# Performance work log

Hardware: AMD Instinct MI355X
Metric: run time of the kernel (lower is better)

The kernel has to match this reference:

```python
import jax, jax.numpy as jnp
import numpy as np

T, N, E = 6, 50000, 1600000
NFEAT, NHID, NCLASS = 256, 256, 16
SLOPE = 11.0 / 48.0  # eval-mode RReLU: mean of default (lower=1/8, upper=1/3)


def _grcu(H_seq, src, dst, val, Wz, Uz, bz, Wr, Ur, br, Wh, Uh, bh, Q0):
    """One GRCU layer: matrix-GRU weight evolution + sparse GCN aggregation per step.
    H_seq: [T, N, in]  src/dst: [T, E] int  val: [T, E]  Q0: [in, out]."""
    n = H_seq.shape[1]

    def step(Q, xs):
        H, s, d, v = xs
        # mat_GRU_cell: x = hidden = prev_Q (z_topk path is unused in this repo's forward)
        z = jax.nn.sigmoid(Wz @ Q + Uz @ Q + bz)
        r = jax.nn.sigmoid(Wr @ Q + Ur @ Q + br)
        h = jnp.tanh(Wh @ Q + Uh @ (r * Q) + bh)
        Qn = (1.0 - z) * Q + z * h
        XW = H @ Qn                                   # [N, out]
        msg = v[:, None] * XW[s]                      # per-edge gather: Ahat row weights
        agg = jax.ops.segment_sum(msg, d, num_segments=n)  # Ahat @ (H @ Qn)
        out = jnp.where(agg >= 0, agg, SLOPE * agg)   # RReLU (eval)
        return Qn, out

    _, out_seq = jax.lax.scan(step, Q0, (H_seq, src, dst, val))
    return out_seq  # [T, N, out]


def setup_inputs() -> dict:
    key = jax.random.key(0)
    ks = iter(jax.random.split(key, 64))

    def rn(shape, scale=0.05):
        return jax.random.normal(next(ks), shape, dtype=jnp.float32) * scale

    inp = {
        "node_feats": jax.random.normal(next(ks), (T, N, NFEAT), dtype=jnp.float32),
        "edge_val": jax.random.uniform(next(ks), (T, E), dtype=jnp.float32),
    }
    for l, (fi, fo) in enumerate([(NFEAT, NHID), (NHID, NHID)]):
        for g in ("z", "r", "h"):
            inp[f"l{l}_W{g}"] = rn((fi, fi))
            inp[f"l{l}_U{g}"] = rn((fi, fi))
            inp[f"l{l}_b{g}"] = jnp.zeros((fi, fo), dtype=jnp.float32)
        inp[f"l{l}_Q0"] = rn((fi, fo))
    inp["mlp_W1"] = rn((NHID, NHID))
    inp["mlp_b1"] = jnp.zeros((NHID,), dtype=jnp.float32)
    inp["mlp_W2"] = rn((NHID, NCLASS))
    inp["mlp_b2"] = jnp.zeros((NCLASS,), dtype=jnp.float32)
    inp["edge_src"] = jax.random.randint(next(ks), (T, E), 0, N, dtype=jnp.int32)
    inp["edge_dst"] = jax.random.randint(next(ks), (T, E), 0, N, dtype=jnp.int32)
    return inp


def reference(node_feats, edge_val,
              l0_Wz, l0_Uz, l0_bz, l0_Wr, l0_Ur, l0_br, l0_Wh, l0_Uh, l0_bh, l0_Q0,
              l1_Wz, l1_Uz, l1_bz, l1_Wr, l1_Ur, l1_br, l1_Wh, l1_Uh, l1_bh, l1_Q0,
              mlp_W1, mlp_b1, mlp_W2, mlp_b2,
              edge_src, edge_dst):
    h1 = _grcu(node_feats, edge_src, edge_dst, edge_val,
               l0_Wz, l0_Uz, l0_bz, l0_Wr, l0_Ur, l0_br, l0_Wh, l0_Uh, l0_bh, l0_Q0)
    h2 = _grcu(h1, edge_src, edge_dst, edge_val,
               l1_Wz, l1_Uz, l1_bz, l1_Wr, l1_Ur, l1_br, l1_Wh, l1_Uh, l1_bh, l1_Q0)
    out = h2[-1]                                    # last timestep, [N, nhid]
    hid = jax.nn.relu(out @ mlp_W1 + mlp_b1)
    logits = hid @ mlp_W2 + mlp_b2
    return jax.nn.log_softmax(logits, axis=1)       # [N, nclass]
```

## Files before the change

### kernel.cpp

```cpp
#include <hip/hip_runtime.h>
#include <cstddef>

#define SLOPE_F (11.0f / 48.0f)

static const int NN = 50000;
static const int EE = 1600000;
static const int D  = 256;
static const int NCH = 196;
static const int GB  = 391;

typedef __attribute__((ext_vector_type(8))) short short8;
typedef __attribute__((ext_vector_type(4))) float f32x4;

__device__ __forceinline__ ushort f2bf(float f) {
    unsigned u = __float_as_uint(f);
    unsigned r = (u + 0x7fffu + ((u >> 16) & 1u)) >> 16;
    return (ushort)r;
}
__device__ __forceinline__ float bf2f(ushort u) {
    return __uint_as_float(((unsigned)u) << 16);
}

__global__ __launch_bounds__(256) void prephist_kernel(
        const float* __restrict__ Wz0, const float* __restrict__ Uz0,
        const float* __restrict__ Wr0, const float* __restrict__ Ur0,
        const float* __restrict__ Wh0, const float* __restrict__ Uh0,
        const float* __restrict__ Wz1, const float* __restrict__ Uz1,
        const float* __restrict__ Wr1, const float* __restrict__ Ur1,
        const float* __restrict__ Wh1, const float* __restrict__ Uh1,
        const float* __restrict__ W1,
        float* __restrict__ TW, ushort* __restrict__ BtW1,
        const int* __restrict__ dst, int* __restrict__ deg) {
    int b = blockIdx.x;
    int tid = threadIdx.x;
    if (b >= 144) {
        int e = (b - 144) * 256 + tid;
        if (e < EE) atomicAdd(&deg[dst[e]], 1);
        return;
    }
    __shared__ float lt[64][65];
    if (b < 128) {
        int mat = b >> 4;
        int tr = (b >> 2) & 3, tc = b & 3;
        const float* P = nullptr; const float* S = nullptr;
        switch (mat) {
            case 0: P = Wz0; S = Uz0; break;
            case 1: P = Wr0; S = Ur0; break;
            case 2: P = Wh0; break;
            case 3: P = Uh0; break;
            case 4: P = Wz1; S = Uz1; break;
            case 5: P = Wr1; S = Ur1; break;
            case 6: P = Wh1; break;
            default: P = Uh1; break;
        }
#pragma unroll
        for (int r0 = 0; r0 < 64; r0 += 4) {
            int r = r0 + (tid >> 6);
            int c = tid & 63;
            int row = tr * 64 + r, col = tc * 64 + c;
            float v = P[row * 256 + col];
            if (S) v += S[row * 256 + col];
            lt[r][c] = v;
        }
        __syncthreads();
#pragma unroll
        for (int c0 = 0; c0 < 64; c0 += 4) {
            int c = c0 + (tid >> 6);
            int r = tid & 63;
            int row = tr * 64 + r, col = tc * 64 + c;
            TW[((size_t)mat * 256 + col) * 256 + row] = lt[r][c];
        }
    } else {
        int t = b - 128;
        int tr = (t >> 2) & 3, tc = t & 3;
#pragma unroll
        for (int r0 = 0; r0 < 64; r0 += 4) {
            int r = r0 + (tid >> 6);
            int c = tid & 63;
            lt[r][c] = W1[(tr * 64 + r) * 256 + tc * 64 + c];
        }
        __syncthreads();
#pragma unroll
        for (int c0 = 0; c0 < 64; c0 += 4) {
            int c = c0 + (tid >> 6);
            int r = tid & 63;
            BtW1[(size_t)(tc * 64 + c) * 256 + tr * 64 + r] = f2bf(lt[r][c]);
        }
    }
}

__global__ __launch_bounds__(256) void gruscan_kernel(
        const float* __restrict__ TW,
        const float* __restrict__ bz0, const float* __restrict__ br0,
        const float* __restrict__ bh0, const float* __restrict__ Q00,
        const float* __restrict__ bz1, const float* __restrict__ br1,
        const float* __restrict__ bh1, const float* __restrict__ Q01,
        ushort* __restrict__ Bt,
        const int* __restrict__ deg, int* __restrict__ rs, int* __restrict__ cur,
        int* __restrict__ bsum, int* __restrict__ boff, int* __restrict__ done) {
    int tid = threadIdx.x;
    if (blockIdx.x >= 128) {
        __shared__ int wsum[4];
        __shared__ int lastflag;
        int blk = blockIdx.x - 128;
        int i = blk * 256 + tid;
        int lane = tid & 63, wv = tid >> 6;
        int v = (i < NN) ? deg[i] : 0;
        int x = v;
#pragma unroll
        for (int off = 1; off < 64; off <<= 1) {
            int t = __shfl_up(x, off, 64);
            if (lane >= off) x += t;
        }
        if (lane == 63) wsum[wv] = x;
        __syncthreads();
        if (tid == 0) {
            int s = 0;
#pragma unroll
            for (int q = 0; q < 4; ++q) { int t = wsum[q]; wsum[q] = s; s += t; }
            bsum[blk] = s;
        }
        __syncthreads();
        if (i < NN) { int p = wsum[wv] + x - v; rs[i] = p; cur[i] = p; }
        __threadfence();
        if (tid == 0) lastflag = (atomicAdd(done, 1) == NCH - 1);
        __syncthreads();
        if (lastflag) {
            __threadfence();
            int bv = (tid < NCH) ? bsum[tid] : 0;
            int bx = bv;
#pragma unroll
            for (int off = 1; off < 64; off <<= 1) {
                int t = __shfl_up(bx, off, 64);
                if (lane >= off) bx += t;
            }
            if (lane == 63) wsum[wv] = bx;
            __syncthreads();
            if (tid == 0) {
                int s = 0;
#pragma unroll
                for (int q = 0; q < 4; ++q) { int t = wsum[q]; wsum[q] = s; s += t; }
            }
            __syncthreads();
            if (tid < NCH) boff[tid] = wsum[wv] + bx - bv;
        }
        return;
    }
    __shared__ float qs[256][4];
    __shared__ float rqs[256][4];
    int layer = blockIdx.x >> 6;
    int j0 = (blockIdx.x & 63) * 4;
    int i = tid;
    const float* MzT = TW + (size_t)layer * 4 * 65536;
    const float* MrT = MzT + 65536;
    const float* WhT = MzT + 2 * 65536;
    const float* UhT = MzT + 3 * 65536;
    const float* bz = layer ? bz1 : bz0;
    const float* br = layer ? br1 : br0;
    const float* bh = layer ? bh1 : bh0;
    const float* Q0 = layer ? Q01 : Q00;

    float4 bzv = *(const float4*)&bz[i * 256 + j0];
    float4 brv = *(const float4*)&br[i * 256 + j0];
    float4 bhv = *(const float4*)&bh[i * 256 + j0];
    float bza[4] = {bzv.x, bzv.y, bzv.z, bzv.w};
    float bra[4] = {brv.x, brv.y, brv.z, brv.w};
    float bha[4] = {bhv.x, bhv.y, bhv.z, bhv.w};

    float4 qv = *(const float4*)&Q0[i * 256 + j0];
    *(float4*)&qs[i][0] = qv;
    __syncthreads();

    float qn[4] = {qv.x, qv.y, qv.z, qv.w};
    for (int step = 0; step < 6; ++step) {
        float az[4] = {}, ar[4] = {}, ah[4] = {};
#pragma unroll 4
        for (int k = 0; k < 256; ++k) {
            float mz = MzT[k * 256 + i];
            float mr = MrT[k * 256 + i];
            float wh = WhT[k * 256 + i];
            float4 qk = *(const float4*)&qs[k][0];
            float qa[4] = {qk.x, qk.y, qk.z, qk.w};
#pragma unroll
            for (int c = 0; c < 4; ++c) {
                az[c] += mz * qa[c];
                ar[c] += mr * qa[c];
                ah[c] += wh * qa[c];
            }
        }
        float z[4], qo[4];
        float4 qown = *(const float4*)&qs[i][0];
        qo[0] = qown.x; qo[1] = qown.y; qo[2] = qown.z; qo[3] = qown.w;
        float rq[4];
#pragma unroll
        for (int c = 0; c < 4; ++c) {
            z[c] = 1.f / (1.f + expf(-(az[c] + bza[c])));
            float r = 1.f / (1.f + expf(-(ar[c] + bra[c])));
            rq[c] = r * qo[c];
        }
        float4 rqv; rqv.x = rq[0]; rqv.y = rq[1]; rqv.z = rq[2]; rqv.w = rq[3];
        *(float4*)&rqs[i][0] = rqv;
        __syncthreads();
        float bu[4] = {};
#pragma unroll 4
        for (int k = 0; k < 256; ++k) {
            float uh = UhT[k * 256 + i];
            float4 rk = *(const float4*)&rqs[k][0];
            float ra[4] = {rk.x, rk.y, rk.z, rk.w};
#pragma unroll
            for (int c = 0; c < 4; ++c) bu[c] += uh * ra[c];
        }
        float4 qnv;
#pragma unroll
        for (int c = 0; c < 4; ++c) {
            float h = tanhf(ah[c] + bu[c] + bha[c]);
            qn[c] = (1.f - z[c]) * qo[c] + z[c] * h;
        }
        qnv.x = qn[0]; qnv.y = qn[1]; qnv.z = qn[2]; qnv.w = qn[3];
        *(float4*)&qs[i][0] = qnv;
        __syncthreads();
    }
#pragma unroll
    for (int c = 0; c < 4; ++c)
        Bt[(size_t)layer * 65536 + (size_t)(j0 + c) * 256 + i] = f2bf(qn[c]);
}

template <int ASRC, int EPI>
__device__ __forceinline__ void gemm_body(int bid, int tid,
                                          const ushort* __restrict__ A,
                                          const float* __restrict__ Af,
                                          const ushort* __restrict__ Bt,
                                          const float* __restrict__ bias,
                                          ushort* __restrict__ C, int M) {
    int w = tid >> 6, l = tid & 63;
    int lr = l & 15;
    int lk = l >> 4;
    int row0 = bid * 128 + w * 32;
    int ra = row0 + lr;      if (ra > M - 1) ra = M - 1;
    int rb = row0 + 16 + lr; if (rb > M - 1) rb = M - 1;
    const ushort* Ap0  = A  + (size_t)ra * 256 + lk * 8;
    const ushort* Ap1  = A  + (size_t)rb * 256 + lk * 8;
    const float*  Apf0 = Af + (size_t)ra * 256 + lk * 8;
    const float*  Apf1 = Af + (size_t)rb * 256 + lk * 8;
    const ushort* Bp   = Bt + (size_t)lr * 256 + lk * 8;

    f32x4 acc0[16] = {};
    f32x4 acc1[16] = {};
#pragma unroll
    for (int kc = 0; kc < 8; ++kc) {
        short8 a0, a1;
        if (ASRC == 0) {
            a0 = *(const short8*)(Ap0 + kc * 32);
            a1 = *(const short8*)(Ap1 + kc * 32);
        } else {
            float4 f0 = *(const float4*)(Apf0 + kc * 32);
            float4 f1 = *(const float4*)(Apf0 + kc * 32 + 4);
            float4 g0 = *(const float4*)(Apf1 + kc * 32);
            float4 g1 = *(const float4*)(Apf1 + kc * 32 + 4);
            a0[0] = (short)f2bf(f0.x); a0[1] = (short)f2bf(f0.y);
            a0[2] = (short)f2bf(f0.z); a0[3] = (short)f2bf(f0.w);
            a0[4] = (short)f2bf(f1.x); a0[5] = (short)f2bf(f1.y);
            a0[6] = (short)f2bf(f1.z); a0[7] = (short)f2bf(f1.w);
            a1[0] = (short)f2bf(g0.x); a1[1] = (short)f2bf(g0.y);
            a1[2] = (short)f2bf(g0.z); a1[3] = (short)f2bf(g0.w);
            a1[4] = (short)f2bf(g1.x); a1[5] = (short)f2bf(g1.y);
            a1[6] = (short)f2bf(g1.z); a1[7] = (short)f2bf(g1.w);
        }
#pragma unroll
        for (int nb = 0; nb < 16; ++nb) {
            short8 bf = *(const short8*)(Bp + (size_t)nb * 4096 + kc * 32);
            acc0[nb] = __builtin_amdgcn_mfma_f32_16x16x32_bf16(a0, bf, acc0[nb], 0, 0, 0);
            acc1[nb] = __builtin_amdgcn_mfma_f32_16x16x32_bf16(a1, bf, acc1[nb], 0, 0, 0);
        }
    }

    int ro = lk * 4;
#pragma unroll
    for (int nb = 0; nb < 16; ++nb) {
        int gc = nb * 16 + lr;
        float bb = (EPI == 1) ? bias[gc] : 0.f;
#pragma unroll
        for (int q = 0; q < 4; ++q) {
            int g0 = row0 + ro + q;
            if (g0 < M) {
                float v = acc0[nb][q];
                if (EPI == 1) v = fmaxf(v + bb, 0.f);
                C[(size_t)g0 * 256 + gc] = f2bf(v);
            }
            int g1 = row0 + 16 + ro + q;
            if (g1 < M) {
                float v = acc1[nb][q];
                if (EPI == 1) v = fmaxf(v + bb, 0.f);
                C[(size_t)g1 * 256 + gc] = f2bf(v);
            }
        }
    }
}

template <int ASRC, int EPI>
__global__ __launch_bounds__(256) void gemm_mfma(const ushort* __restrict__ A,
                                                 const float* __restrict__ Af,
                                                 const ushort* __restrict__ Bt,
                                                 const float* __restrict__ bias,
                                                 ushort* __restrict__ C, int M) {
    gemm_body<ASRC, EPI>(blockIdx.x, threadIdx.x, A, Af, Bt, bias, C, M);
}

__global__ __launch_bounds__(256) void gemsca_kernel(const float* __restrict__ Af,
                                                     const ushort* __restrict__ Bt,
                                                     ushort* __restrict__ C, int M,
                                                     const int* __restrict__ src,
                                                     const int* __restrict__ dst,
                                                     const float* __restrict__ val,
                                                     int* __restrict__ cur,
                                                     const int* __restrict__ boff,
                                                     unsigned long long* __restrict__ csr) {
    if (blockIdx.x < GB) {
        gemm_body<1, 0>(blockIdx.x, threadIdx.x, nullptr, Af, Bt, nullptr, C, M);
        return;
    }
    int e = (blockIdx.x - GB) * 256 + threadIdx.x;
    if (e < EE) {
        int d = dst[e];
        int p = atomicAdd(&cur[d], 1) + boff[d >> 8];
        unsigned long long pk = (unsigned long long)(unsigned)src[e]
                              | ((unsigned long long)(unsigned)__float_as_uint(val[e]) << 32);
        __builtin_nontemporal_store(pk, &csr[p]);
    }
}

__global__ __launch_bounds__(256) void agg_csr_kernel(const ushort* __restrict__ XW,
                                                      const int2* __restrict__ csr,
                                                      const int* __restrict__ rs,
                                                      const int* __restrict__ boff,
                                                      ushort* __restrict__ out) {
    int d = blockIdx.x * 4 + (threadIdx.x >> 6);
    if (d >= NN) return;
    int l = threadIdx.x & 63;
    int h = l >> 5;
    int il = l & 31;
    int beg = rs[d] + boff[d >> 8];
    int end = (d + 1 < NN) ? (rs[d + 1] + boff[(d + 1) >> 8]) : EE;
    float a0 = 0.f, a1 = 0.f, a2 = 0.f, a3 = 0.f;
    float a4 = 0.f, a5 = 0.f, a6 = 0.f, a7 = 0.f;
    int i = beg + h;
    for (; i + 14 < end; i += 16) {
        int2 e[8];
        short8 x[8];
#pragma unroll
        for (int u = 0; u < 8; ++u) e[u] = csr[i + 2 * u];
#pragma unroll
        for (int u = 0; u < 8; ++u)
            x[u] = *(const short8*)&XW[(size_t)e[u].x * D + il * 8];
#pragma unroll
        for (int u = 0; u < 8; ++u) {
            float v = __int_as_float(e[u].y);
            a0 += v * bf2f((ushort)x[u][0]);
            a1 += v * bf2f((ushort)x[u][1]);
            a2 += v * bf2f((ushort)x[u][2]);
            a3 += v * bf2f((ushort)x[u][3]);
            a4 += v * bf2f((ushort)x[u][4]);
            a5 += v * bf2f((ushort)x[u][5]);
            a6 += v * bf2f((ushort)x[u][6]);
            a7 += v * bf2f((ushort)x[u][7]);
        }
    }
    for (; i + 6 < end; i += 8) {
        int2 e[4];
        short8 x[4];
#pragma unroll
        for (int u = 0; u < 4; ++u) e[u] = csr[i + 2 * u];
#pragma unroll
        for (int u = 0; u < 4; ++u)
            x[u] = *(const short8*)&XW[(size_t)e[u].x * D + il * 8];
#pragma unroll
        for (int u = 0; u < 4; ++u) {
            float v = __int_as_float(e[u].y);
            a0 += v * bf2f((ushort)x[u][0]);
            a1 += v * bf2f((ushort)x[u][1]);
            a2 += v * bf2f((ushort)x[u][2]);
            a3 += v * bf2f((ushort)x[u][3]);
            a4 += v * bf2f((ushort)x[u][4]);
            a5 += v * bf2f((ushort)x[u][5]);
            a6 += v * bf2f((ushort)x[u][6]);
            a7 += v * bf2f((ushort)x[u][7]);
        }
    }
    for (; i < end; i += 2) {
        int2 e0 = csr[i];
        float v0 = __int_as_float(e0.y);
        short8 x0 = *(const short8*)&XW[(size_t)e0.x * D + il * 8];
        a0 += v0 * bf2f((ushort)x0[0]); a1 += v0 * bf2f((ushort)x0[1]);
        a2 += v0 * bf2f((ushort)x0[2]); a3 += v0 * bf2f((ushort)x0[3]);
        a4 += v0 * bf2f((ushort)x0[4]); a5 += v0 * bf2f((ushort)x0[5]);
        a6 += v0 * bf2f((ushort)x0[6]); a7 += v0 * bf2f((ushort)x0[7]);
    }
    a0 += __shfl_xor(a0, 32); a1 += __shfl_xor(a1, 32);
    a2 += __shfl_xor(a2, 32); a3 += __shfl_xor(a3, 32);
    a4 += __shfl_xor(a4, 32); a5 += __shfl_xor(a5, 32);
    a6 += __shfl_xor(a6, 32); a7 += __shfl_xor(a7, 32);
    if (h == 0) {
        float r[8] = {a0, a1, a2, a3, a4, a5, a6, a7};
        short8 o;
#pragma unroll
        for (int c = 0; c < 8; ++c) {
            float v = r[c];
            v = (v >= 0.f) ? v : SLOPE_F * v;
            o[c] = (short)f2bf(v);
        }
        *(short8*)&out[(size_t)d * D + il * 8] = o;
    }
}

__global__ void mlp2_kernel(const ushort* __restrict__ hid, const float* __restrict__ W2,
                            const float* __restrict__ b2, float* __restrict__ out, int M) {
    int tid = threadIdx.x;
    int n = blockIdx.x * 16 + (tid >> 4);
    int c = tid & 15;
    if (n >= M) return;
    float acc = b2[c];
    const ushort* hp = hid + (size_t)n * D;
    for (int k = 0; k < D; k += 8) {
        short8 h8 = *(const short8*)(hp + k);
#pragma unroll
        for (int u = 0; u < 8; ++u)
            acc += bf2f((ushort)h8[u]) * W2[(k + u) * 16 + c];
    }
    float m = acc;
#pragma unroll
    for (int off = 1; off < 16; off <<= 1)
        m = fmaxf(m, __shfl_xor(m, off, 16));
    float ex = expf(acc - m);
    float s = ex;
#pragma unroll
    for (int off = 1; off < 16; off <<= 1)
        s += __shfl_xor(s, off, 16);
    out[(size_t)n * 16 + c] = acc - m - logf(s);
}

extern "C" void kernel_launch(void* const* d_in, const int* in_sizes, int n_in,
                              void* d_out, int out_size, void* d_ws, size_t ws_size,
                              hipStream_t stream) {
    const float* node_feats = (const float*)d_in[0];
    const float* edge_val   = (const float*)d_in[1];
    const float* l0_Wz = (const float*)d_in[2];
    const float* l0_Uz = (const float*)d_in[3];
    const float* l0_bz = (const float*)d_in[4];
    const float* l0_Wr = (const float*)d_in[5];
    const float* l0_Ur = (const float*)d_in[6];
    const float* l0_br = (const float*)d_in[7];
    const float* l0_Wh = (const float*)d_in[8];
    const float* l0_Uh = (const float*)d_in[9];
    const float* l0_bh = (const float*)d_in[10];
    const float* l0_Q0 = (const float*)d_in[11];
    const float* l1_Wz = (const float*)d_in[12];
    const float* l1_Uz = (const float*)d_in[13];
    const float* l1_bz = (const float*)d_in[14];
    const float* l1_Wr = (const float*)d_in[15];
    const float* l1_Ur = (const float*)d_in[16];
    const float* l1_br = (const float*)d_in[17];
    const float* l1_Wh = (const float*)d_in[18];
    const float* l1_Uh = (const float*)d_in[19];
    const float* l1_bh = (const float*)d_in[20];
    const float* l1_Q0 = (const float*)d_in[21];
    const float* W1 = (const float*)d_in[22];
    const float* b1 = (const float*)d_in[23];
    const float* W2 = (const float*)d_in[24];
    const float* b2 = (const float*)d_in[25];
    const int* e_src = (const int*)d_in[26];
    const int* e_dst = (const int*)d_in[27];
    float* out = (float*)d_out;

    const size_t BIG = (size_t)NN * D;
    ushort* XWb = (ushort*)d_ws;
    ushort* H   = XWb + BIG;
    ushort* Bt  = H + BIG;
    float*  TW  = (float*)(Bt + 3 * 65536);
    int2*   csr = (int2*)(TW + 8 * 65536);
    int*    deg = (int*)(csr + EE);
    int*    done = deg + NN;
    int*    rs  = done + 1;
    int*    cur = rs + NN;
    int*    bsum = cur + NN;
    int*    boff = bsum + 200;

    const float* feats5 = node_feats + (size_t)5 * BIG;
    const int*   src5   = e_src + (size_t)5 * EE;
    const int*   dst5   = e_dst + (size_t)5 * EE;
    const float* val5   = edge_val + (size_t)5 * EE;

    hipMemsetAsync(deg, 0, (NN + 1) * sizeof(int), stream);

    const int histblocks = (EE + 255) / 256;
    prephist_kernel<<<144 + histblocks, 256, 0, stream>>>(
        l0_Wz, l0_Uz, l0_Wr, l0_Ur, l0_Wh, l0_Uh,
        l1_Wz, l1_Uz, l1_Wr, l1_Ur, l1_Wh, l1_Uh,
        W1, TW, Bt + 2 * 65536, dst5, deg);

    gruscan_kernel<<<128 + NCH, 256, 0, stream>>>(TW, l0_bz, l0_br, l0_bh, l0_Q0,
                                                  l1_bz, l1_br, l1_bh, l1_Q0, Bt,
                                                  deg, rs, cur, bsum, boff, done);

    gemsca_kernel<<<GB + histblocks, 256, 0, stream>>>(feats5, Bt + 0 * 65536, XWb, NN,
                                                       src5, dst5, val5, cur, boff,
                                                       (unsigned long long*)csr);

    const int ablocks = (NN + 3) / 4;

    agg_csr_kernel<<<ablocks, 256, 0, stream>>>(XWb, csr, rs, boff, H);

    gemm_mfma<0, 0><<<GB, 256, 0, stream>>>(H, nullptr, Bt + 1 * 65536, nullptr, XWb, NN);
    agg_csr_kernel<<<ablocks, 256, 0, stream>>>(XWb, csr, rs, boff, H);

    gemm_mfma<0, 1><<<GB, 256, 0, stream>>>(H, nullptr, Bt + 2 * 65536, b1, XWb, NN);
    mlp2_kernel<<<(NN + 15) / 16, 256, 0, stream>>>(XWb, W2, b2, out, NN);
}
```

Baseline: 714.3 us.

## Rewrite matrix-GRU weight scan with bf16 MFMA and grid-wide barriers

The per-thread fp32 scalar FMA loops in the GRU weight-evolution kernel are replaced with 16x16x32 bf16 MFMA tiles. Each weight matrix is split into hi and lo bf16 halves so the weights keep roughly fp32 accuracy. The recurrent Q and r*Q state now live in global bf16 buffers and are exchanged between 128 blocks through a spin-wait grid barrier, two per step. The aim is to cut the latency-bound serial GRU phase. The cost is lower precision on the recurrent state and a reliance on all 128 GRU blocks being co-resident for the barrier.

```diff
diff --git a/kernel.cpp b/kernel.cpp
--- a/kernel.cpp
+++ b/kernel.cpp
@@ -29,19 +29,18 @@
         const float* __restrict__ Wr1, const float* __restrict__ Ur1,
         const float* __restrict__ Wh1, const float* __restrict__ Uh1,
         const float* __restrict__ W1,
-        float* __restrict__ TW, ushort* __restrict__ BtW1,
+        const float* __restrict__ Q00, const float* __restrict__ Q01,
+        ushort* __restrict__ WB, ushort* __restrict__ BtW1, ushort* __restrict__ Qt,
         const int* __restrict__ dst, int* __restrict__ deg) {
     int b = blockIdx.x;
     int tid = threadIdx.x;
-    if (b >= 144) {
-        int e = (b - 144) * 256 + tid;
+    if (b >= 112) {
+        int e = (b - 112) * 256 + tid;
         if (e < EE) atomicAdd(&deg[dst[e]], 1);
         return;
     }
-    __shared__ float lt[64][65];
-    if (b < 128) {
-        int mat = b >> 4;
-        int tr = (b >> 2) & 3, tc = b & 3;
+    if (b < 64) {
+        int mat = b >> 3;
         const float* P = nullptr; const float* S = nullptr;
         switch (mat) {
             case 0: P = Wz0; S = Uz0; break;
@@ -53,25 +52,22 @@
             case 6: P = Wh1; break;
             default: P = Uh1; break;
         }
-#pragma unroll
-        for (int r0 = 0; r0 < 64; r0 += 4) {
-            int r = r0 + (tid >> 6);
-            int c = tid & 63;
-            int row = tr * 64 + r, col = tc * 64 + c;
-            float v = P[row * 256 + col];
-            if (S) v += S[row * 256 + col];
-            lt[r][c] = v;
-        }
-        __syncthreads();
-#pragma unroll
-        for (int c0 = 0; c0 < 64; c0 += 4) {
-            int c = c0 + (tid >> 6);
-            int r = tid & 63;
-            int row = tr * 64 + r, col = tc * 64 + c;
-            TW[((size_t)mat * 256 + col) * 256 + row] = lt[r][c];
-        }
-    } else {
-        int t = b - 128;
+        size_t base = (size_t)mat * 2 * 65536;
+#pragma unroll 4
+        for (int u = 0; u < 32; ++u) {
+            int idx = (b & 7) * 8192 + u * 256 + tid;
+            float v = P[idx];
+            if (S) v += S[idx];
+            ushort hi = f2bf(v);
+            ushort lo = f2bf(v - bf2f(hi));
+            WB[base + idx] = hi;
+            WB[base + 65536 + idx] = lo;
+        }
+        return;
+    }
+    __shared__ float lt[64][65];
+    if (b < 80) {
+        int t = b - 64;
         int tr = (t >> 2) & 3, tc = t & 3;
 #pragma unroll
         for (int r0 = 0; r0 < 64; r0 += 4) {
@@ -86,16 +82,47 @@
             int r = tid & 63;
             BtW1[(size_t)(tc * 64 + c) * 256 + tr * 64 + r] = f2bf(lt[r][c]);
         }
-    }
-}
-
-__global__ __launch_bounds__(256) void gruscan_kernel(
-        const float* __restrict__ TW,
+    } else {
+        int t = b - 80;
+        int layer = t >> 4;
+        int tt = t & 15;
+        int tr = (tt >> 2) & 3, tc = tt & 3;
+        const float* Q0 = layer ? Q01 : Q00;
+#pragma unroll
+        for (int r0 = 0; r0 < 64; r0 += 4) {
+            int r = r0 + (tid >> 6);
+            int c = tid & 63;
+            lt[r][c] = Q0[(tr * 64 + r) * 256 + tc * 64 + c];
+        }
+        __syncthreads();
+#pragma unroll
+        for (int c0 = 0; c0 < 64; c0 += 4) {
+            int c = c0 + (tid >> 6);
+            int r = tid & 63;
+            Qt[(size_t)layer * 65536 + (size_t)(tc * 64 + c) * 256 + tr * 64 + r] =
+                f2bf(lt[r][c]);
+        }
+    }
+}
+
+__device__ __forceinline__ void gridbar(int* __restrict__ bar, int idx, int nb) {
+    __threadfence();
+    __syncthreads();
+    if (threadIdx.x == 0) {
+        atomicAdd(&bar[idx], 1);
+        while (atomicAdd(&bar[idx], 0) < nb) { __builtin_amdgcn_s_sleep(8); }
+        __threadfence();
+    }
+    __syncthreads();
+}
+
+__global__ __launch_bounds__(256, 2) void grubar_kernel(
+        const ushort* __restrict__ WB,
         const float* __restrict__ bz0, const float* __restrict__ br0,
-        const float* __restrict__ bh0, const float* __restrict__ Q00,
+        const float* __restrict__ bh0,
         const float* __restrict__ bz1, const float* __restrict__ br1,
-        const float* __restrict__ bh1, const float* __restrict__ Q01,
-        ushort* __restrict__ Bt,
+        const float* __restrict__ bh1,
+        ushort* __restrict__ Qt, ushort* __restrict__ RQt, int* __restrict__ bar,
         const int* __restrict__ deg, int* __restrict__ rs, int* __restrict__ cur,
         int* __restrict__ bsum, int* __restrict__ boff, int* __restrict__ done) {
     int tid = threadIdx.x;
@@ -146,83 +173,96 @@
         }
         return;
     }
-    __shared__ float qs[256][4];
-    __shared__ float rqs[256][4];
-    int layer = blockIdx.x >> 6;
-    int j0 = (blockIdx.x & 63) * 4;
-    int i = tid;
-    const float* MzT = TW + (size_t)layer * 4 * 65536;
-    const float* MrT = MzT + 65536;
-    const float* WhT = MzT + 2 * 65536;
-    const float* UhT = MzT + 3 * 65536;
+    int wid = blockIdx.x * 4 + (tid >> 6);
+    int l = tid & 63;
+    int layer = wid >> 8;
+    int t = wid & 255;
+    int i0 = (t >> 4) * 16;
+    int j0 = (t & 15) * 16;
+    int lr = l & 15, lk = l >> 4;
+    int ro = lk * 4;
+
+    const ushort* Wz = WB + ((size_t)layer * 4 + 0) * 2 * 65536;
+    const ushort* Wr = WB + ((size_t)layer * 4 + 1) * 2 * 65536;
+    const ushort* Wh = WB + ((size_t)layer * 4 + 2) * 2 * 65536;
+    const ushort* Wu = WB + ((size_t)layer * 4 + 3) * 2 * 65536;
+    ushort* Qtl  = Qt  + (size_t)layer * 65536;
+    ushort* RQtl = RQt + (size_t)layer * 65536;
     const float* bz = layer ? bz1 : bz0;
     const float* br = layer ? br1 : br0;
     const float* bh = layer ? bh1 : bh0;
-    const float* Q0 = layer ? Q01 : Q00;
-
-    float4 bzv = *(const float4*)&bz[i * 256 + j0];
-    float4 brv = *(const float4*)&br[i * 256 + j0];
-    float4 bhv = *(const float4*)&bh[i * 256 + j0];
-    float bza[4] = {bzv.x, bzv.y, bzv.z, bzv.w};
-    float bra[4] = {brv.x, brv.y, brv.z, brv.w};
-    float bha[4] = {bhv.x, bhv.y, bhv.z, bhv.w};
-
-    float4 qv = *(const float4*)&Q0[i * 256 + j0];
-    *(float4*)&qs[i][0] = qv;
-    __syncthreads();
-
-    float qn[4] = {qv.x, qv.y, qv.z, qv.w};
+
+    float bza[4], bra[4], bha[4];
+#pragma unroll
+    for (int q = 0; q < 4; ++q) {
+        int i = i0 + ro + q;
+        bza[q] = bz[i * 256 + j0 + lr];
+        bra[q] = br[i * 256 + j0 + lr];
+        bha[q] = bh[i * 256 + j0 + lr];
+    }
+
+    const int afo = (i0 + lr) * 256 + lk * 8;
+    const int bfo = (j0 + lr) * 256 + lk * 8;
+    const int qo  = (j0 + lr) * 256 + i0 + ro;
+
     for (int step = 0; step < 6; ++step) {
-        float az[4] = {}, ar[4] = {}, ah[4] = {};
-#pragma unroll 4
-        for (int k = 0; k < 256; ++k) {
-            float mz = MzT[k * 256 + i];
-            float mr = MrT[k * 256 + i];
-            float wh = WhT[k * 256 + i];
-            float4 qk = *(const float4*)&qs[k][0];
-            float qa[4] = {qk.x, qk.y, qk.z, qk.w};
-#pragma unroll
-            for (int c = 0; c < 4; ++c) {
-                az[c] += mz * qa[c];
-                ar[c] += mr * qa[c];
-                ah[c] += wh * qa[c];
-            }
-        }
-        float z[4], qo[4];
-        float4 qown = *(const float4*)&qs[i][0];
-        qo[0] = qown.x; qo[1] = qown.y; qo[2] = qown.z; qo[3] = qown.w;
-        float rq[4];
-#pragma unroll
-        for (int c = 0; c < 4; ++c) {
-            z[c] = 1.f / (1.f + expf(-(az[c] + bza[c])));
-            float r = 1.f / (1.f + expf(-(ar[c] + bra[c])));
-            rq[c] = r * qo[c];
-        }
-        float4 rqv; rqv.x = rq[0]; rqv.y = rq[1]; rqv.z = rq[2]; rqv.w = rq[3];
-        *(float4*)&rqs[i][0] = rqv;
-        __syncthreads();
-        float bu[4] = {};
-#pragma unroll 4
-        for (int k = 0; k < 256; ++k) {
-            float uh = UhT[k * 256 + i];
-            float4 rk = *(const float4*)&rqs[k][0];
-            float ra[4] = {rk.x, rk.y, rk.z, rk.w};
-#pragma unroll
-            for (int c = 0; c < 4; ++c) bu[c] += uh * ra[c];
-        }
-        float4 qnv;
-#pragma unroll
-        for (int c = 0; c < 4; ++c) {
-            float h = tanhf(ah[c] + bu[c] + bha[c]);
-            qn[c] = (1.f - z[c]) * qo[c] + z[c] * h;
-        }
-        qnv.x = qn[0]; qnv.y = qn[1]; qnv.z = qn[2]; qnv.w = qn[3];
-        *(float4*)&qs[i][0] = qnv;
-        __syncthreads();
-    }
-#pragma unroll
-    for (int c = 0; c < 4; ++c)
-        Bt[(size_t)layer * 65536 + (size_t)(j0 + c) * 256 + i] = f2bf(qn[c]);
+        f32x4 az = {}, ar = {}, ah = {};
+#pragma unroll
+        for (int kc = 0; kc < 8; ++kc) {
+            short8 qf  = *(const short8*)&Qtl[bfo + kc * 32];
+            short8 wzh = *(const short8*)&Wz[afo + kc * 32];
+            short8 wzl = *(const short8*)&Wz[65536 + afo + kc * 32];
+            az = __builtin_amdgcn_mfma_f32_16x16x32_bf16(wzh, qf, az, 0, 0, 0);
+            az = __builtin_amdgcn_mfma_f32_16x16x32_bf16(wzl, qf, az, 0, 0, 0);
+            short8 wrh = *(const short8*)&Wr[afo + kc * 32];
+            short8 wrl = *(const short8*)&Wr[65536 + afo + kc * 32];
+            ar = __builtin_amdgcn_mfma_f32_16x16x32_bf16(wrh, qf, ar, 0, 0, 0);
+            ar = __builtin_amdgcn_mfma_f32_16x16x32_bf16(wrl, qf, ar, 0, 0, 0);
+            short8 whh = *(const short8*)&Wh[afo + kc * 32];
+            short8 whl = *(const short8*)&Wh[65536 + afo + kc * 32];
+            ah = __builtin_amdgcn_mfma_f32_16x16x32_bf16(whh, qf, ah, 0, 0, 0);
+            ah = __builtin_amdgcn_mfma_f32_16x16x32_bf16(whl, qf, ah, 0, 0, 0);
+        }
+        ushort4 qv4 = *(const ushort4*)&Qtl[qo];
+        float qv[4] = {bf2f(qv4.x), bf2f(qv4.y), bf2f(qv4.z), bf2f(qv4.w)};
+        float zz[4];
+        ushort4 rq4;
+        {
+            float rr0 = 1.f / (1.f + expf(-(ar[0] + bra[0])));
+            float rr1 = 1.f / (1.f + expf(-(ar[1] + bra[1])));
+            float rr2 = 1.f / (1.f + expf(-(ar[2] + bra[2])));
+            float rr3 = 1.f / (1.f + expf(-(ar[3] + bra[3])));
+            zz[0] = 1.f / (1.f + expf(-(az[0] + bza[0])));
+            zz[1] = 1.f / (1.f + expf(-(az[1] + bza[1])));
+            zz[2] = 1.f / (1.f + expf(-(az[2] + bza[2])));
+            zz[3] = 1.f / (1.f + expf(-(az[3] + bza[3])));
+            rq4.x = f2bf(rr0 * qv[0]);
+            rq4.y = f2bf(rr1 * qv[1]);
+            rq4.z = f2bf(rr2 * qv[2]);
+            rq4.w = f2bf(rr3 * qv[3]);
+        }
+        *(ushort4*)&RQtl[qo] = rq4;
+        gridbar(bar, step * 2, 128);
+
+        f32x4 au = {};
+#pragma unroll
+        for (int kc = 0; kc < 8; ++kc) {
+            short8 rf  = *(const short8*)&RQtl[bfo + kc * 32];
+            short8 wuh = *(const short8*)&Wu[afo + kc * 32];
+            short8 wul = *(const short8*)&Wu[65536 + afo + kc * 32];
+            au = __builtin_amdgcn_mfma_f32_16x16x32_bf16(wuh, rf, au, 0, 0, 0);
+            au = __builtin_amdgcn_mfma_f32_16x16x32_bf16(wul, rf, au, 0, 0, 0);
+        }
+        ushort4 qn4;
+#pragma unroll
+        for (int q = 0; q < 4; ++q) {
+            float h = tanhf(ah[q] + au[q] + bha[q]);
+            float qn = (1.f - zz[q]) * qv[q] + zz[q] * h;
+            ((ushort*)&qn4)[q] = f2bf(qn);
+        }
+        *(ushort4*)&Qtl[qo] = qn4;
+        if (step < 5) gridbar(bar, step * 2 + 1, 128);
+    }
 }
 
 template <int ASRC, int EPI>
@@ -475,11 +515,13 @@
     ushort* XWb = (ushort*)d_ws;
     ushort* H   = XWb + BIG;
     ushort* Bt  = H + BIG;
-    float*  TW  = (float*)(Bt + 3 * 65536);
-    int2*   csr = (int2*)(TW + 8 * 65536);
+    ushort* RQt = Bt + 3 * 65536;
+    ushort* WB  = RQt + 2 * 65536;
+    int2*   csr = (int2*)(WB + 16 * 65536);
     int*    deg = (int*)(csr + EE);
     int*    done = deg + NN;
-    int*    rs  = done + 1;
+    int*    bar  = done + 1;
+    int*    rs  = bar + 12;
     int*    cur = rs + NN;
     int*    bsum = cur + NN;
     int*    boff = bsum + 200;
@@ -489,17 +531,18 @@
     const int*   dst5   = e_dst + (size_t)5 * EE;
     const float* val5   = edge_val + (size_t)5 * EE;
 
-    hipMemsetAsync(deg, 0, (NN + 1) * sizeof(int), stream);
+    hipMemsetAsync(deg, 0, (NN + 13) * sizeof(int), stream);
 
     const int histblocks = (EE + 255) / 256;
-    prephist_kernel<<<144 + histblocks, 256, 0, stream>>>(
+    prephist_kernel<<<112 + histblocks, 256, 0, stream>>>(
         l0_Wz, l0_Uz, l0_Wr, l0_Ur, l0_Wh, l0_Uh,
         l1_Wz, l1_Uz, l1_Wr, l1_Ur, l1_Wh, l1_Uh,
-        W1, TW, Bt + 2 * 65536, dst5, deg);
-
-    gruscan_kernel<<<128 + NCH, 256, 0, stream>>>(TW, l0_bz, l0_br, l0_bh, l0_Q0,
-                                                  l1_bz, l1_br, l1_bh, l1_Q0, Bt,
-                                                  deg, rs, cur, bsum, boff, done);
+        W1, l0_Q0, l1_Q0, WB, Bt + 2 * 65536, Bt, dst5, deg);
+
+    grubar_kernel<<<128 + NCH, 256, 0, stream>>>(WB, l0_bz, l0_br, l0_bh,
+                                                 l1_bz, l1_br, l1_bh,
+                                                 Bt, RQt, bar,
+                                                 deg, rs, cur, bsum, boff, done);
 
     gemsca_kernel<<<GB + histblocks, 256, 0, stream>>>(feats5, Bt + 0 * 65536, XWb, NN,
                                                        src5, dst5, val5, cur, boff,
```

After: 843.9 us. +18.1%, slower.
